# Performance work log

Hardware: AMD Instinct MI355X
Metric: run time of the kernel (lower is better)

The kernel has to match this reference:

```python
import jax, jax.numpy as jnp
import numpy as np

N_USERS = 100000
EMBED = 128
N_EDGES = 1_600_000  # avg degree 16


def setup_inputs() -> dict:
    key = jax.random.key(0)
    k1, k2, k3, k4, k5 = jax.random.split(key, 5)
    s_rows = jnp.sort(jax.random.randint(k1, (N_EDGES,), 0, N_USERS))
    s_cols = jax.random.randint(k2, (N_EDGES,), 0, N_USERS)
    # row-normalization D^-1 A, matching the scipy preprocessing in __init__
    deg = jax.ops.segment_sum(jnp.ones((N_EDGES,), jnp.float32), s_rows, num_segments=N_USERS)
    deg = jnp.where(deg == 0, 1.0, deg)
    s_values = 1.0 / deg[s_rows]
    user_embeds = jax.random.normal(k3, (N_USERS, EMBED), jnp.float32) * 0.1
    bound = float(np.sqrt(6.0 / (EMBED + EMBED)))  # xavier_uniform
    W0 = jax.random.uniform(k4, (EMBED, EMBED), jnp.float32, -bound, bound)
    W1 = jax.random.uniform(k5, (EMBED, EMBED), jnp.float32, -bound, bound)
    return {"user_embeds": user_embeds, "s_rows": s_rows, "s_cols": s_cols,
            "s_values": s_values, "W0": W0, "W1": W1}


def reference(user_embeds, s_rows, s_cols, s_values, W0, W1):
    # SocialGCN.forward: per layer x_new = x + dropout(S @ (x @ W_l));
    # dropout is identity in eval mode. Returns all layer outputs (stacked).
    n_users = user_embeds.shape[0]
    outs = [user_embeds]
    x = user_embeds
    for W in (W0, W1):
        xt = x @ W  # [n_users, d] dense GEMM
        # SpMM: out[r] = sum_{e: rows[e]==r} vals[e] * xt[cols[e]]
        msg = s_values[:, None] * xt[s_cols]  # [n_edges, d] irregular gather
        agg = jax.ops.segment_sum(msg, s_rows, num_segments=n_users)
        x = x + agg  # residual add
        outs.append(x)
    return jnp.stack(outs)  # [n_layers+1, n_users, d]
```

## Files before the change

### kernel.cpp

```cpp
#include <hip/hip_runtime.h>

#define N_USERS 100000
#define EMBED   128

typedef __attribute__((ext_vector_type(8))) short bf16x8;
typedef __attribute__((ext_vector_type(4))) float f32x4;

__global__ __launch_bounds__(256) void rowptr_kernel(const int* __restrict__ rows,
                                                     int* __restrict__ row_ptr,
                                                     int n_rows, int n_edges) {
  int r = blockIdx.x * blockDim.x + threadIdx.x;
  if (r > n_rows) return;
  int lo = 0, hi = n_edges;
  while (lo < hi) {
    int mid = (lo + hi) >> 1;
    if (rows[mid] < r) lo = mid + 1; else hi = mid;
  }
  row_ptr[r] = lo;
}

__global__ __launch_bounds__(256) void wconv_kernel(const float* __restrict__ W0,
                                                    const float* __restrict__ W1,
                                                    uint* __restrict__ Wt0,
                                                    uint* __restrict__ Wt1) {
  const float* W  = blockIdx.x ? W1 : W0;
  uint*        Wt = blockIdx.x ? Wt1 : Wt0;
  for (int idx = threadIdx.x; idx < 128 * 64; idx += 256) {
    int n = idx >> 6;
    int kp = idx & 63;
    float a = W[(2 * kp) * 128 + n];
    float b = W[(2 * kp + 1) * 128 + n];
    uint o;
    asm("v_cvt_pk_bf16_f32 %0, %1, %2" : "=v"(o) : "v"(a), "v"(b));
    Wt[n * 64 + kp] = o;
  }
}

__global__ __launch_bounds__(256) void gemm_kernel(const float* __restrict__ X,
                                                   const ushort* __restrict__ Wt,
                                                   ushort* __restrict__ Y,
                                                   float* __restrict__ Xcopy) {
  const int tid  = threadIdx.x;
  const int wave = tid >> 6;
  const int lane = tid & 63;
  const int l15  = lane & 15;
  const int lg   = lane >> 4;
  const int m    = blockIdx.x * 64 + wave * 16 + l15;
  const int mc   = m < N_USERS ? m : N_USERS - 1;
  const bool act = m < N_USERS;
  const float* xrow = X + (size_t)mc * EMBED;

  f32x4 acc[8];
  #pragma unroll
  for (int t = 0; t < 8; ++t) acc[t] = (f32x4){0.f, 0.f, 0.f, 0.f};

  #pragma unroll
  for (int s = 0; s < 4; ++s) {
    const int k0 = s * 32 + lg * 8;
    float4 xa = *(const float4*)(xrow + k0);
    float4 xb = *(const float4*)(xrow + k0 + 4);
    if (Xcopy && act) {
      *(float4*)(Xcopy + (size_t)m * EMBED + k0)     = xa;
      *(float4*)(Xcopy + (size_t)m * EMBED + k0 + 4) = xb;
    }
    union { bf16x8 v; uint u[4]; } bfr;
    asm("v_cvt_pk_bf16_f32 %0, %1, %2" : "=v"(bfr.u[0]) : "v"(xa.x), "v"(xa.y));
    asm("v_cvt_pk_bf16_f32 %0, %1, %2" : "=v"(bfr.u[1]) : "v"(xa.z), "v"(xa.w));
    asm("v_cvt_pk_bf16_f32 %0, %1, %2" : "=v"(bfr.u[2]) : "v"(xb.x), "v"(xb.y));
    asm("v_cvt_pk_bf16_f32 %0, %1, %2" : "=v"(bfr.u[3]) : "v"(xb.z), "v"(xb.w));
    #pragma unroll
    for (int nt = 0; nt < 8; ++nt) {
      union { bf16x8 v; uint4 u; } afr;
      afr.u = *(const uint4*)(Wt + (size_t)(nt * 16 + l15) * 128 + k0);
      acc[nt] = __builtin_amdgcn_mfma_f32_16x16x32_bf16(afr.v, bfr.v, acc[nt], 0, 0, 0);
    }
  }

  if (act) {
    ushort* yrow = Y + (size_t)m * EMBED;
    #pragma unroll
    for (int nt = 0; nt < 8; ++nt) {
      uint2 o;
      asm("v_cvt_pk_bf16_f32 %0, %1, %2" : "=v"(o.x) : "v"(acc[nt][0]), "v"(acc[nt][1]));
      asm("v_cvt_pk_bf16_f32 %0, %1, %2" : "=v"(o.y) : "v"(acc[nt][2]), "v"(acc[nt][3]));
      *(uint2*)(yrow + nt * 16 + lg * 4) = o;
    }
  }
}

#define FMA8(g, v)                                                     \
  do {                                                                 \
    acc[0] = fmaf((v), __uint_as_float((g).x << 16),         acc[0]);  \
    acc[1] = fmaf((v), __uint_as_float((g).x & 0xffff0000u), acc[1]);  \
    acc[2] = fmaf((v), __uint_as_float((g).y << 16),         acc[2]);  \
    acc[3] = fmaf((v), __uint_as_float((g).y & 0xffff0000u), acc[3]);  \
    acc[4] = fmaf((v), __uint_as_float((g).z << 16),         acc[4]);  \
    acc[5] = fmaf((v), __uint_as_float((g).z & 0xffff0000u), acc[5]);  \
    acc[6] = fmaf((v), __uint_as_float((g).w << 16),         acc[6]);  \
    acc[7] = fmaf((v), __uint_as_float((g).w & 0xffff0000u), acc[7]);  \
  } while (0)

__global__ __launch_bounds__(256) void spmm_kernel(const ushort* __restrict__ XT,
                                                   const float* __restrict__ X,
                                                   const int* __restrict__ row_ptr,
                                                   const int* __restrict__ cols,
                                                   const float* __restrict__ vals,
                                                   float* __restrict__ OUT) {
  const int tid = threadIdx.x;
  const int l   = tid & 15;
  const int rg  = tid >> 4;
  const int row = blockIdx.x * 16 + rg;
  if (row >= N_USERS) return;
  const int start = row_ptr[row];
  const int end   = row_ptr[row + 1];
  const uint4* XT4 = (const uint4*)XT;

  float acc[8];
  {
    float4 r0 = *(const float4*)(X + (size_t)row * EMBED + l * 8);
    float4 r1 = *(const float4*)(X + (size_t)row * EMBED + l * 8 + 4);
    acc[0] = r0.x; acc[1] = r0.y; acc[2] = r0.z; acc[3] = r0.w;
    acc[4] = r1.x; acc[5] = r1.y; acc[6] = r1.z; acc[7] = r1.w;
  }

  int e = start;
  int e_pre = (start + 3) & ~3;
  if (e_pre > end) e_pre = end;
  for (; e < e_pre; ++e) {
    int   c = cols[e];
    float v = vals[e];
    uint4 g = XT4[(size_t)c * 16 + l];
    FMA8(g, v);
  }
  for (; e + 4 <= end; e += 4) {
    int4   c = *(const int4*)(cols + e);
    float4 v = *(const float4*)(vals + e);
    uint4 g0 = XT4[(size_t)c.x * 16 + l];
    uint4 g1 = XT4[(size_t)c.y * 16 + l];
    uint4 g2 = XT4[(size_t)c.z * 16 + l];
    uint4 g3 = XT4[(size_t)c.w * 16 + l];
    FMA8(g0, v.x);
    FMA8(g1, v.y);
    FMA8(g2, v.z);
    FMA8(g3, v.w);
  }
  for (; e < end; ++e) {
    int   c = cols[e];
    float v = vals[e];
    uint4 g = XT4[(size_t)c * 16 + l];
    FMA8(g, v);
  }

  float4 o0 = {acc[0], acc[1], acc[2], acc[3]};
  float4 o1 = {acc[4], acc[5], acc[6], acc[7]};
  *(float4*)(OUT + (size_t)row * EMBED + l * 8)     = o0;
  *(float4*)(OUT + (size_t)row * EMBED + l * 8 + 4) = o1;
}

extern "C" void kernel_launch(void* const* d_in, const int* in_sizes, int n_in,
                              void* d_out, int out_size, void* d_ws, size_t ws_size,
                              hipStream_t stream) {
  const float* user_embeds = (const float*)d_in[0];
  const int*   s_rows      = (const int*)d_in[1];
  const int*   s_cols      = (const int*)d_in[2];
  const float* s_values    = (const float*)d_in[3];
  const float* W0          = (const float*)d_in[4];
  const float* W1          = (const float*)d_in[5];
  float* out = (float*)d_out;

  const int n_edges = in_sizes[1];
  const size_t layer = (size_t)N_USERS * EMBED;

  char* ws = (char*)d_ws;
  ushort* xt      = (ushort*)ws;   ws += layer * sizeof(ushort);
  ushort* Wt0     = (ushort*)ws;   ws += 128 * 128 * sizeof(ushort);
  ushort* Wt1     = (ushort*)ws;   ws += 128 * 128 * sizeof(ushort);
  int*    row_ptr = (int*)ws;

  rowptr_kernel<<<(N_USERS + 1 + 255) / 256, 256, 0, stream>>>(
      s_rows, row_ptr, N_USERS, n_edges);
  wconv_kernel<<<2, 256, 0, stream>>>(W0, W1, (uint*)Wt0, (uint*)Wt1);

  const ushort* Wtl[2] = {Wt0, Wt1};
  for (int l = 0; l < 2; ++l) {
    const float* Xl = (l == 0) ? user_embeds : (out + l * layer);
    gemm_kernel<<<(N_USERS + 63) / 64, 256, 0, stream>>>(
        Xl, Wtl[l], xt, l == 0 ? out : nullptr);
    spmm_kernel<<<(N_USERS + 15) / 16, 256, 0, stream>>>(
        xt, Xl, row_ptr, s_cols, s_values, out + (l + 1) * layer);
  }
}
```

Measured before the change: 239.5 us.

## Split bf16 XT into four column-quarter planes and run SpMM per quarter

The GEMM now writes its bf16 output as four separate planes of 32 columns each. The SpMM runs as four launches, one per plane, with four lanes per row. Each gather plane is 6.4 MB, small enough to stay resident in L2 or the infinite cache during random column gathers. The cost is re-reading row_ptr, cols and vals four times, three extra launches, and less memory-level parallelism per row.

```diff
diff --git a/kernel.cpp b/kernel.cpp
--- a/kernel.cpp
+++ b/kernel.cpp
@@ -2,6 +2,7 @@
 
 #define N_USERS 100000
 #define EMBED   128
+#define QSTRIDE ((size_t)N_USERS * 32)
 
 typedef __attribute__((ext_vector_type(8))) short bf16x8;
 typedef __attribute__((ext_vector_type(4))) float f32x4;
@@ -77,13 +78,14 @@
   }
 
   if (act) {
-    ushort* yrow = Y + (size_t)m * EMBED;
     #pragma unroll
     for (int nt = 0; nt < 8; ++nt) {
       uint2 o;
       asm("v_cvt_pk_bf16_f32 %0, %1, %2" : "=v"(o.x) : "v"(acc[nt][0]), "v"(acc[nt][1]));
       asm("v_cvt_pk_bf16_f32 %0, %1, %2" : "=v"(o.y) : "v"(acc[nt][2]), "v"(acc[nt][3]));
-      *(uint2*)(yrow + nt * 16 + lg * 4) = o;
+      ushort* dst = Y + (size_t)(nt >> 1) * QSTRIDE + (size_t)m * 32
+                      + ((nt & 1) * 16 + lg * 4);
+      *(uint2*)dst = o;
     }
   }
 }
@@ -100,25 +102,27 @@
     acc[7] = fmaf((v), __uint_as_float((g).w & 0xffff0000u), acc[7]);  \
   } while (0)
 
-__global__ __launch_bounds__(256) void spmm_kernel(const ushort* __restrict__ XT,
-                                                   const float* __restrict__ X,
-                                                   const int* __restrict__ row_ptr,
-                                                   const int* __restrict__ cols,
-                                                   const float* __restrict__ vals,
-                                                   float* __restrict__ OUT) {
+__global__ __launch_bounds__(256) void spmm_q_kernel(const ushort* __restrict__ XTq,
+                                                     const float* __restrict__ X,
+                                                     const int* __restrict__ row_ptr,
+                                                     const int* __restrict__ cols,
+                                                     const float* __restrict__ vals,
+                                                     float* __restrict__ OUT,
+                                                     int q) {
   const int tid = threadIdx.x;
-  const int l   = tid & 15;
-  const int rg  = tid >> 4;
-  const int row = blockIdx.x * 16 + rg;
+  const int l   = tid & 3;
+  const int g   = tid >> 2;
+  const int row = blockIdx.x * 64 + g;
   if (row >= N_USERS) return;
   const int start = row_ptr[row];
   const int end   = row_ptr[row + 1];
-  const uint4* XT4 = (const uint4*)XT;
+  const uint4* XT4 = (const uint4*)XTq;
 
   float acc[8];
+  const float* xr = X + (size_t)row * EMBED + q * 32 + l * 8;
   {
-    float4 r0 = *(const float4*)(X + (size_t)row * EMBED + l * 8);
-    float4 r1 = *(const float4*)(X + (size_t)row * EMBED + l * 8 + 4);
+    float4 r0 = *(const float4*)xr;
+    float4 r1 = *(const float4*)(xr + 4);
     acc[0] = r0.x; acc[1] = r0.y; acc[2] = r0.z; acc[3] = r0.w;
     acc[4] = r1.x; acc[5] = r1.y; acc[6] = r1.z; acc[7] = r1.w;
   }
@@ -129,16 +133,16 @@
   for (; e < e_pre; ++e) {
     int   c = cols[e];
     float v = vals[e];
-    uint4 g = XT4[(size_t)c * 16 + l];
-    FMA8(g, v);
+    uint4 gt = XT4[(size_t)c * 4 + l];
+    FMA8(gt, v);
   }
   for (; e + 4 <= end; e += 4) {
     int4   c = *(const int4*)(cols + e);
     float4 v = *(const float4*)(vals + e);
-    uint4 g0 = XT4[(size_t)c.x * 16 + l];
-    uint4 g1 = XT4[(size_t)c.y * 16 + l];
-    uint4 g2 = XT4[(size_t)c.z * 16 + l];
-    uint4 g3 = XT4[(size_t)c.w * 16 + l];
+    uint4 g0 = XT4[(size_t)c.x * 4 + l];
+    uint4 g1 = XT4[(size_t)c.y * 4 + l];
+    uint4 g2 = XT4[(size_t)c.z * 4 + l];
+    uint4 g3 = XT4[(size_t)c.w * 4 + l];
     FMA8(g0, v.x);
     FMA8(g1, v.y);
     FMA8(g2, v.z);
@@ -147,14 +151,15 @@
   for (; e < end; ++e) {
     int   c = cols[e];
     float v = vals[e];
-    uint4 g = XT4[(size_t)c * 16 + l];
-    FMA8(g, v);
-  }
-
+    uint4 gt = XT4[(size_t)c * 4 + l];
+    FMA8(gt, v);
+  }
+
+  float* orow = OUT + (size_t)row * EMBED + q * 32 + l * 8;
   float4 o0 = {acc[0], acc[1], acc[2], acc[3]};
   float4 o1 = {acc[4], acc[5], acc[6], acc[7]};
-  *(float4*)(OUT + (size_t)row * EMBED + l * 8)     = o0;
-  *(float4*)(OUT + (size_t)row * EMBED + l * 8 + 4) = o1;
+  *(float4*)orow       = o0;
+  *(float4*)(orow + 4) = o1;
 }
 
 extern "C" void kernel_launch(void* const* d_in, const int* in_sizes, int n_in,
@@ -186,7 +191,10 @@
     const float* Xl = (l == 0) ? user_embeds : (out + l * layer);
     gemm_kernel<<<(N_USERS + 63) / 64, 256, 0, stream>>>(
         Xl, Wtl[l], xt, l == 0 ? out : nullptr);
-    spmm_kernel<<<(N_USERS + 15) / 16, 256, 0, stream>>>(
-        xt, Xl, row_ptr, s_cols, s_values, out + (l + 1) * layer);
-  }
-}
+    for (int q = 0; q < 4; ++q) {
+      spmm_q_kernel<<<(N_USERS + 63) / 64, 256, 0, stream>>>(
+          xt + (size_t)q * QSTRIDE, Xl, row_ptr, s_cols, s_values,
+          out + (l + 1) * layer, q);
+    }
+  }
+}
```

Measured after the change: 336.5 us. 1.4x slower.

## Bucket edges by column range and process SpMM in phases for cache locality

Applied to the files above, without the earlier changes.

Adds a preprocessing kernel that reorders each row's edges into 8 column buckets, each covering 12500 source rows of the transformed embedding. The new SpMM kernel gives each block 100 rows, holds 7 rows of accumulators per thread, and walks the buckets phase by phase. Blocks running at the same time then gather from a similar slice of XT, which should raise L2/MALL hit rates. The cost is a serial per-row bucketing pass with 8 scans over each row's edges, more registers per thread, and only 1000 blocks, which lowers parallelism.

```diff
diff --git a/kernel.cpp b/kernel.cpp
--- a/kernel.cpp
+++ b/kernel.cpp
@@ -1,10 +1,15 @@
 #include <hip/hip_runtime.h>
 
-#define N_USERS 100000
-#define EMBED   128
+#define N_USERS  100000
+#define EMBED    128
+#define NPHASE   8
+#define BUCKETW  12500
+#define RPB      100
+#define NBLK     1000
 
 typedef __attribute__((ext_vector_type(8))) short bf16x8;
 typedef __attribute__((ext_vector_type(4))) float f32x4;
+typedef __attribute__((ext_vector_type(4))) uint  u32x4;
 
 __global__ __launch_bounds__(256) void rowptr_kernel(const int* __restrict__ rows,
                                                      int* __restrict__ row_ptr,
@@ -17,6 +22,27 @@
     if (rows[mid] < r) lo = mid + 1; else hi = mid;
   }
   row_ptr[r] = lo;
+}
+
+__global__ __launch_bounds__(256) void bucket_kernel(const int* __restrict__ row_ptr,
+                                                     const int* __restrict__ cols,
+                                                     const float* __restrict__ vals,
+                                                     int* __restrict__ rp2,
+                                                     int* __restrict__ cols2,
+                                                     float* __restrict__ vals2) {
+  int r = blockIdx.x * blockDim.x + threadIdx.x;
+  if (r >= N_USERS) return;
+  const int s = row_ptr[r], e = row_ptr[r + 1];
+  int w = s;
+  #pragma unroll
+  for (int p = 0; p < NPHASE; ++p) {
+    rp2[9 * r + p] = w;
+    for (int i = s; i < e; ++i) {
+      int c = cols[i];
+      if (c / BUCKETW == p) { cols2[w] = c; vals2[w] = vals[i]; ++w; }
+    }
+  }
+  rp2[9 * r + 8] = e;
 }
 
 __global__ __launch_bounds__(256) void wconv_kernel(const float* __restrict__ W0,
@@ -88,73 +114,75 @@
   }
 }
 
-#define FMA8(g, v)                                                     \
-  do {                                                                 \
-    acc[0] = fmaf((v), __uint_as_float((g).x << 16),         acc[0]);  \
-    acc[1] = fmaf((v), __uint_as_float((g).x & 0xffff0000u), acc[1]);  \
-    acc[2] = fmaf((v), __uint_as_float((g).y << 16),         acc[2]);  \
-    acc[3] = fmaf((v), __uint_as_float((g).y & 0xffff0000u), acc[3]);  \
-    acc[4] = fmaf((v), __uint_as_float((g).z << 16),         acc[4]);  \
-    acc[5] = fmaf((v), __uint_as_float((g).z & 0xffff0000u), acc[5]);  \
-    acc[6] = fmaf((v), __uint_as_float((g).w << 16),         acc[6]);  \
-    acc[7] = fmaf((v), __uint_as_float((g).w & 0xffff0000u), acc[7]);  \
-  } while (0)
-
-__global__ __launch_bounds__(256) void spmm_kernel(const ushort* __restrict__ XT,
-                                                   const float* __restrict__ X,
-                                                   const int* __restrict__ row_ptr,
-                                                   const int* __restrict__ cols,
-                                                   const float* __restrict__ vals,
-                                                   float* __restrict__ OUT) {
-  const int tid = threadIdx.x;
-  const int l   = tid & 15;
-  const int rg  = tid >> 4;
-  const int row = blockIdx.x * 16 + rg;
-  if (row >= N_USERS) return;
-  const int start = row_ptr[row];
-  const int end   = row_ptr[row + 1];
-  const uint4* XT4 = (const uint4*)XT;
-
-  float acc[8];
-  {
-    float4 r0 = *(const float4*)(X + (size_t)row * EMBED + l * 8);
-    float4 r1 = *(const float4*)(X + (size_t)row * EMBED + l * 8 + 4);
-    acc[0] = r0.x; acc[1] = r0.y; acc[2] = r0.z; acc[3] = r0.w;
-    acc[4] = r1.x; acc[5] = r1.y; acc[6] = r1.z; acc[7] = r1.w;
-  }
-
-  int e = start;
-  int e_pre = (start + 3) & ~3;
-  if (e_pre > end) e_pre = end;
-  for (; e < e_pre; ++e) {
-    int   c = cols[e];
-    float v = vals[e];
-    uint4 g = XT4[(size_t)c * 16 + l];
-    FMA8(g, v);
-  }
-  for (; e + 4 <= end; e += 4) {
-    int4   c = *(const int4*)(cols + e);
-    float4 v = *(const float4*)(vals + e);
-    uint4 g0 = XT4[(size_t)c.x * 16 + l];
-    uint4 g1 = XT4[(size_t)c.y * 16 + l];
-    uint4 g2 = XT4[(size_t)c.z * 16 + l];
-    uint4 g3 = XT4[(size_t)c.w * 16 + l];
-    FMA8(g0, v.x);
-    FMA8(g1, v.y);
-    FMA8(g2, v.z);
-    FMA8(g3, v.w);
-  }
-  for (; e < end; ++e) {
-    int   c = cols[e];
-    float v = vals[e];
-    uint4 g = XT4[(size_t)c * 16 + l];
-    FMA8(g, v);
-  }
-
-  float4 o0 = {acc[0], acc[1], acc[2], acc[3]};
-  float4 o1 = {acc[4], acc[5], acc[6], acc[7]};
-  *(float4*)(OUT + (size_t)row * EMBED + l * 8)     = o0;
-  *(float4*)(OUT + (size_t)row * EMBED + l * 8 + 4) = o1;
+__device__ __forceinline__ void fma8(float* acc, u32x4 g, float v) {
+  acc[0] = fmaf(v, __uint_as_float(g[0] << 16),         acc[0]);
+  acc[1] = fmaf(v, __uint_as_float(g[0] & 0xffff0000u), acc[1]);
+  acc[2] = fmaf(v, __uint_as_float(g[1] << 16),         acc[2]);
+  acc[3] = fmaf(v, __uint_as_float(g[1] & 0xffff0000u), acc[3]);
+  acc[4] = fmaf(v, __uint_as_float(g[2] << 16),         acc[4]);
+  acc[5] = fmaf(v, __uint_as_float(g[2] & 0xffff0000u), acc[5]);
+  acc[6] = fmaf(v, __uint_as_float(g[3] << 16),         acc[6]);
+  acc[7] = fmaf(v, __uint_as_float(g[3] & 0xffff0000u), acc[7]);
+}
+
+__global__ __launch_bounds__(256, 4) void spmm_phased(const ushort* __restrict__ XT,
+                                                      const float* __restrict__ X,
+                                                      const int* __restrict__ rp2,
+                                                      const int* __restrict__ cols2,
+                                                      const float* __restrict__ vals2,
+                                                      float* __restrict__ OUT) {
+  const int tid  = threadIdx.x;
+  const int l    = tid & 15;
+  const int g    = tid >> 4;
+  const int base = blockIdx.x * RPB;
+  const u32x4* XT4 = (const u32x4*)XT;
+
+  float acc[7][8];
+  #pragma unroll
+  for (int i = 0; i < 7; ++i)
+    #pragma unroll
+    for (int j = 0; j < 8; ++j) acc[i][j] = 0.f;
+
+  for (int p = 0; p < NPHASE; ++p) {
+    #pragma unroll
+    for (int i = 0; i < 7; ++i) {
+      if (g + 16 * i < RPB) {
+        const int r = base + g + 16 * i;
+        const int s = rp2[9 * r + p];
+        const int e = rp2[9 * r + p + 1];
+        int e2 = s;
+        for (; e2 + 2 <= e; e2 += 2) {
+          int   c0 = cols2[e2],   c1 = cols2[e2 + 1];
+          float v0 = vals2[e2],   v1 = vals2[e2 + 1];
+          u32x4 g0 = XT4[(size_t)c0 * 16 + l];
+          u32x4 g1 = XT4[(size_t)c1 * 16 + l];
+          fma8(acc[i], g0, v0);
+          fma8(acc[i], g1, v1);
+        }
+        if (e2 < e) {
+          u32x4 g0 = XT4[(size_t)cols2[e2] * 16 + l];
+          fma8(acc[i], g0, vals2[e2]);
+        }
+      }
+    }
+  }
+
+  #pragma unroll
+  for (int i = 0; i < 7; ++i) {
+    if (g + 16 * i < RPB) {
+      const int r = base + g + 16 * i;
+      const float* xr = X + (size_t)r * EMBED + l * 8;
+      float4 r0 = *(const float4*)xr;
+      float4 r1 = *(const float4*)(xr + 4);
+      float4 o0 = {acc[i][0] + r0.x, acc[i][1] + r0.y,
+                   acc[i][2] + r0.z, acc[i][3] + r0.w};
+      float4 o1 = {acc[i][4] + r1.x, acc[i][5] + r1.y,
+                   acc[i][6] + r1.z, acc[i][7] + r1.w};
+      float* orow = OUT + (size_t)r * EMBED + l * 8;
+      *(float4*)orow       = o0;
+      *(float4*)(orow + 4) = o1;
+    }
+  }
 }
 
 extern "C" void kernel_launch(void* const* d_in, const int* in_sizes, int n_in,
@@ -172,21 +200,26 @@
   const size_t layer = (size_t)N_USERS * EMBED;
 
   char* ws = (char*)d_ws;
-  ushort* xt      = (ushort*)ws;   ws += layer * sizeof(ushort);
-  ushort* Wt0     = (ushort*)ws;   ws += 128 * 128 * sizeof(ushort);
-  ushort* Wt1     = (ushort*)ws;   ws += 128 * 128 * sizeof(ushort);
-  int*    row_ptr = (int*)ws;
+  ushort* xt      = (ushort*)ws;  ws += layer * sizeof(ushort);
+  ushort* Wt0     = (ushort*)ws;  ws += 128 * 128 * sizeof(ushort);
+  ushort* Wt1     = (ushort*)ws;  ws += 128 * 128 * sizeof(ushort);
+  int*    row_ptr = (int*)ws;     ws += (N_USERS + 1) * sizeof(int) + 12;
+  int*    rp2     = (int*)ws;     ws += (size_t)9 * N_USERS * sizeof(int);
+  int*    cols2   = (int*)ws;     ws += (size_t)n_edges * sizeof(int);
+  float*  vals2   = (float*)ws;
 
   rowptr_kernel<<<(N_USERS + 1 + 255) / 256, 256, 0, stream>>>(
       s_rows, row_ptr, N_USERS, n_edges);
   wconv_kernel<<<2, 256, 0, stream>>>(W0, W1, (uint*)Wt0, (uint*)Wt1);
+  bucket_kernel<<<(N_USERS + 255) / 256, 256, 0, stream>>>(
+      row_ptr, s_cols, s_values, rp2, cols2, vals2);
 
   const ushort* Wtl[2] = {Wt0, Wt1};
   for (int l = 0; l < 2; ++l) {
     const float* Xl = (l == 0) ? user_embeds : (out + l * layer);
     gemm_kernel<<<(N_USERS + 63) / 64, 256, 0, stream>>>(
         Xl, Wtl[l], xt, l == 0 ? out : nullptr);
-    spmm_kernel<<<(N_USERS + 15) / 16, 256, 0, stream>>>(
-        xt, Xl, row_ptr, s_cols, s_values, out + (l + 1) * layer);
-  }
-}
+    spmm_phased<<<NBLK, 256, 0, stream>>>(
+        xt, Xl, rp2, cols2, vals2, out + (l + 1) * layer);
+  }
+}
```

Result: slower. 441.4 us (+84.3%).

## Quantize GEMM output to per-row int8 to halve SpMM gather traffic

Applied to the files above, without the earlier changes.

The GEMM epilogue now quantizes each output row to offset uint8 with a per-row absmax scale, replacing the bf16 store. The SpMM gathers 128-byte int8 rows instead of 256-byte bf16 rows. It folds the scale into the edge weight, converts bytes with v_cvt_f32_ubyte, and removes the +128 offset using the accumulated weight sum. Each row is now handled by 8 lanes with 16 accumulators instead of 16 lanes with 8, to cut random-gather bandwidth. The cost is lower precision (about 7 bits), which may break accuracy tolerance, plus an extra per-edge scale load.

```diff
diff --git a/kernel.cpp b/kernel.cpp
--- a/kernel.cpp
+++ b/kernel.cpp
@@ -1,7 +1,7 @@
 #include <hip/hip_runtime.h>
 
-#define N_USERS 100000
-#define EMBED   128
+#define N_USERS  100000
+#define EMBED    128
 
 typedef __attribute__((ext_vector_type(8))) short bf16x8;
 typedef __attribute__((ext_vector_type(4))) float f32x4;
@@ -38,7 +38,8 @@
 
 __global__ __launch_bounds__(256) void gemm_kernel(const float* __restrict__ X,
                                                    const ushort* __restrict__ Wt,
-                                                   ushort* __restrict__ Y,
+                                                   unsigned char* __restrict__ Y8,
+                                                   float* __restrict__ scale_arr,
                                                    float* __restrict__ Xcopy) {
   const int tid  = threadIdx.x;
   const int wave = tid >> 6;
@@ -77,84 +78,107 @@
   }
 
   if (act) {
-    ushort* yrow = Y + (size_t)m * EMBED;
+    float amax = 0.f;
+    #pragma unroll
+    for (int nt = 0; nt < 8; ++nt)
+      #pragma unroll
+      for (int i = 0; i < 4; ++i) amax = fmaxf(amax, fabsf(acc[nt][i]));
+    amax = fmaxf(amax, __shfl_xor(amax, 16));
+    amax = fmaxf(amax, __shfl_xor(amax, 32));
+    const float inv = amax > 0.f ? 127.0f / amax : 0.f;
+    if (lg == 0) scale_arr[m] = amax * (1.0f / 127.0f);
+
+    unsigned char* yrow = Y8 + (size_t)m * EMBED;
     #pragma unroll
     for (int nt = 0; nt < 8; ++nt) {
-      uint2 o;
-      asm("v_cvt_pk_bf16_f32 %0, %1, %2" : "=v"(o.x) : "v"(acc[nt][0]), "v"(acc[nt][1]));
-      asm("v_cvt_pk_bf16_f32 %0, %1, %2" : "=v"(o.y) : "v"(acc[nt][2]), "v"(acc[nt][3]));
-      *(uint2*)(yrow + nt * 16 + lg * 4) = o;
+      uint q = 0;
+      #pragma unroll
+      for (int i = 0; i < 4; ++i) {
+        int qi = __float2int_rn(acc[nt][i] * inv) + 128;
+        q |= (uint)qi << (8 * i);
+      }
+      *(uint*)(yrow + nt * 16 + lg * 4) = q;
     }
   }
 }
 
-#define FMA8(g, v)                                                     \
-  do {                                                                 \
-    acc[0] = fmaf((v), __uint_as_float((g).x << 16),         acc[0]);  \
-    acc[1] = fmaf((v), __uint_as_float((g).x & 0xffff0000u), acc[1]);  \
-    acc[2] = fmaf((v), __uint_as_float((g).y << 16),         acc[2]);  \
-    acc[3] = fmaf((v), __uint_as_float((g).y & 0xffff0000u), acc[3]);  \
-    acc[4] = fmaf((v), __uint_as_float((g).z << 16),         acc[4]);  \
-    acc[5] = fmaf((v), __uint_as_float((g).z & 0xffff0000u), acc[5]);  \
-    acc[6] = fmaf((v), __uint_as_float((g).w << 16),         acc[6]);  \
-    acc[7] = fmaf((v), __uint_as_float((g).w & 0xffff0000u), acc[7]);  \
-  } while (0)
-
-__global__ __launch_bounds__(256) void spmm_kernel(const ushort* __restrict__ XT,
+__device__ __forceinline__ void fma16(float* acc, uint4 g, float vs) {
+  float f;
+  #define CVT_ACC(word, b, slot)                                        \
+    asm("v_cvt_f32_ubyte" #b " %0, %1" : "=v"(f) : "v"(word));          \
+    acc[slot] = fmaf(vs, f, acc[slot]);
+  CVT_ACC(g.x, 0, 0)  CVT_ACC(g.x, 1, 1)  CVT_ACC(g.x, 2, 2)  CVT_ACC(g.x, 3, 3)
+  CVT_ACC(g.y, 0, 4)  CVT_ACC(g.y, 1, 5)  CVT_ACC(g.y, 2, 6)  CVT_ACC(g.y, 3, 7)
+  CVT_ACC(g.z, 0, 8)  CVT_ACC(g.z, 1, 9)  CVT_ACC(g.z, 2, 10) CVT_ACC(g.z, 3, 11)
+  CVT_ACC(g.w, 0, 12) CVT_ACC(g.w, 1, 13) CVT_ACC(g.w, 2, 14) CVT_ACC(g.w, 3, 15)
+  #undef CVT_ACC
+}
+
+__global__ __launch_bounds__(256) void spmm_kernel(const unsigned char* __restrict__ XT8,
+                                                   const float* __restrict__ scale_arr,
                                                    const float* __restrict__ X,
                                                    const int* __restrict__ row_ptr,
                                                    const int* __restrict__ cols,
                                                    const float* __restrict__ vals,
                                                    float* __restrict__ OUT) {
   const int tid = threadIdx.x;
-  const int l   = tid & 15;
-  const int rg  = tid >> 4;
-  const int row = blockIdx.x * 16 + rg;
+  const int l   = tid & 7;
+  const int rg  = tid >> 3;
+  const int row = blockIdx.x * 32 + rg;
   if (row >= N_USERS) return;
   const int start = row_ptr[row];
   const int end   = row_ptr[row + 1];
-  const uint4* XT4 = (const uint4*)XT;
-
-  float acc[8];
-  {
-    float4 r0 = *(const float4*)(X + (size_t)row * EMBED + l * 8);
-    float4 r1 = *(const float4*)(X + (size_t)row * EMBED + l * 8 + 4);
-    acc[0] = r0.x; acc[1] = r0.y; acc[2] = r0.z; acc[3] = r0.w;
-    acc[4] = r1.x; acc[5] = r1.y; acc[6] = r1.z; acc[7] = r1.w;
-  }
+  const uint4* XT4 = (const uint4*)XT8;
+
+  float acc[16];
+  #pragma unroll
+  for (int j = 0; j < 16; ++j) acc[j] = 0.f;
+  float vsum = 0.f;
 
   int e = start;
   int e_pre = (start + 3) & ~3;
   if (e_pre > end) e_pre = end;
   for (; e < e_pre; ++e) {
-    int   c = cols[e];
-    float v = vals[e];
-    uint4 g = XT4[(size_t)c * 16 + l];
-    FMA8(g, v);
+    int c = cols[e];
+    float vs = vals[e] * scale_arr[c];
+    vsum += vs;
+    fma16(acc, XT4[(size_t)c * 8 + l], vs);
   }
   for (; e + 4 <= end; e += 4) {
-    int4   c = *(const int4*)(cols + e);
-    float4 v = *(const float4*)(vals + e);
-    uint4 g0 = XT4[(size_t)c.x * 16 + l];
-    uint4 g1 = XT4[(size_t)c.y * 16 + l];
-    uint4 g2 = XT4[(size_t)c.z * 16 + l];
-    uint4 g3 = XT4[(size_t)c.w * 16 + l];
-    FMA8(g0, v.x);
-    FMA8(g1, v.y);
-    FMA8(g2, v.z);
-    FMA8(g3, v.w);
+    int4   ca = *(const int4*)(cols + e);
+    float4 va = *(const float4*)(vals + e);
+    float s0 = scale_arr[ca.x], s1 = scale_arr[ca.y];
+    float s2 = scale_arr[ca.z], s3 = scale_arr[ca.w];
+    uint4 g0 = XT4[(size_t)ca.x * 8 + l];
+    uint4 g1 = XT4[(size_t)ca.y * 8 + l];
+    uint4 g2 = XT4[(size_t)ca.z * 8 + l];
+    uint4 g3 = XT4[(size_t)ca.w * 8 + l];
+    float vs0 = va.x * s0, vs1 = va.y * s1, vs2 = va.z * s2, vs3 = va.w * s3;
+    vsum += vs0 + vs1 + vs2 + vs3;
+    fma16(acc, g0, vs0);
+    fma16(acc, g1, vs1);
+    fma16(acc, g2, vs2);
+    fma16(acc, g3, vs3);
   }
   for (; e < end; ++e) {
-    int   c = cols[e];
-    float v = vals[e];
-    uint4 g = XT4[(size_t)c * 16 + l];
-    FMA8(g, v);
-  }
-
-  float4 o0 = {acc[0], acc[1], acc[2], acc[3]};
-  float4 o1 = {acc[4], acc[5], acc[6], acc[7]};
-  *(float4*)(OUT + (size_t)row * EMBED + l * 8)     = o0;
-  *(float4*)(OUT + (size_t)row * EMBED + l * 8 + 4) = o1;
+    int c = cols[e];
+    float vs = vals[e] * scale_arr[c];
+    vsum += vs;
+    fma16(acc, XT4[(size_t)c * 8 + l], vs);
+  }
+
+  const float corr = vsum * 128.0f;
+  const float* xr = X + (size_t)row * EMBED + l * 16;
+  float*       orow = OUT + (size_t)row * EMBED + l * 16;
+  #pragma unroll
+  for (int k = 0; k < 4; ++k) {
+    float4 r = *(const float4*)(xr + k * 4);
+    float4 o = {acc[k * 4 + 0] - corr + r.x,
+                acc[k * 4 + 1] - corr + r.y,
+                acc[k * 4 + 2] - corr + r.z,
+                acc[k * 4 + 3] - corr + r.w};
+    *(float4*)(orow + k * 4) = o;
+  }
 }
 
 extern "C" void kernel_launch(void* const* d_in, const int* in_sizes, int n_in,
@@ -172,10 +196,11 @@
   const size_t layer = (size_t)N_USERS * EMBED;
 
   char* ws = (char*)d_ws;
-  ushort* xt      = (ushort*)ws;   ws += layer * sizeof(ushort);
-  ushort* Wt0     = (ushort*)ws;   ws += 128 * 128 * sizeof(ushort);
-  ushort* Wt1     = (ushort*)ws;   ws += 128 * 128 * sizeof(ushort);
-  int*    row_ptr = (int*)ws;
+  unsigned char* xt8 = (unsigned char*)ws;  ws += layer;
+  float*  scale_arr  = (float*)ws;          ws += N_USERS * sizeof(float);
+  ushort* Wt0        = (ushort*)ws;         ws += 128 * 128 * sizeof(ushort);
+  ushort* Wt1        = (ushort*)ws;         ws += 128 * 128 * sizeof(ushort);
+  int*    row_ptr    = (int*)ws;
 
   rowptr_kernel<<<(N_USERS + 1 + 255) / 256, 256, 0, stream>>>(
       s_rows, row_ptr, N_USERS, n_edges);
@@ -185,8 +210,8 @@
   for (int l = 0; l < 2; ++l) {
     const float* Xl = (l == 0) ? user_embeds : (out + l * layer);
     gemm_kernel<<<(N_USERS + 63) / 64, 256, 0, stream>>>(
-        Xl, Wtl[l], xt, l == 0 ? out : nullptr);
-    spmm_kernel<<<(N_USERS + 15) / 16, 256, 0, stream>>>(
-        xt, Xl, row_ptr, s_cols, s_values, out + (l + 1) * layer);
-  }
-}
+        Xl, Wtl[l], xt8, scale_arr, l == 0 ? out : nullptr);
+    spmm_kernel<<<(N_USERS + 31) / 32, 256, 0, stream>>>(
+        xt8, scale_arr, Xl, row_ptr, s_cols, s_values, out + (l + 1) * layer);
+  }
+}
```

Result: faster. 201.1 us (-16.0%).
